# Kernel optimization log

Hardware: AMD Instinct MI355X
Metric: run time of the kernel (lower is better)

Reference implementation:

```python
import jax, jax.numpy as jnp
import numpy as np

C, H, W = 3, 2048, 2048
N_ANN = 64
P = 512  # patch resolution
RESIZE_FRAC = 0.5  # deterministic midpoint of resize_range=(0.25, 0.75)
MIN_SIZE = 10


def setup_inputs() -> dict:
    key = jax.random.key(0)
    k1, k2, k3, k4 = jax.random.split(key, 4)
    image = jax.random.normal(k1, (C, H, W), jnp.float32)
    patch = jax.random.uniform(k2, (C, P, P), jnp.float32)
    # build valid normalized xyxy boxes (x1<x2, y1<y2) inside the image
    centers = jax.random.uniform(k3, (N_ANN, 2), minval=0.2, maxval=0.8)
    sizes = jax.random.uniform(k4, (N_ANN, 2), minval=0.10, maxval=0.30)
    xy1 = jnp.clip(centers - sizes / 2, 0.0, 1.0)
    xy2 = jnp.clip(centers + sizes / 2, 0.0, 1.0)
    annotations = jnp.concatenate([xy1, xy2], axis=1).astype(jnp.float32)  # [N,4] xyxy
    return {"image": image, "annotations": annotations, "patch": patch}


def reference(image, annotations, patch):
    """MODE_CENTER_BBOX forward: for each bbox, bilinearly resize the patch to
    wh x wh (wh = min(bbox_w, bbox_h) * RESIZE_FRAC, >= MIN_SIZE), then paste it
    centered in the bbox (clamped to the image). embed_patch's mask arithmetic
    (image_mask*image + patch_mask*patch) is exactly a region overwrite."""
    c, h, w = image.shape
    # normalized_annotations=True: scale by [W, H, W, H] then floor to long
    ann = np.asarray(annotations * jnp.array([w, h, w, h], jnp.float32)).astype(np.int64)
    img = image
    for x1, y1, x2, y2 in ann:
        bw, bh = int(x2 - x1), int(y2 - y1)
        wh = max(int(min(bw, bh) * RESIZE_FRAC), MIN_SIZE)
        rp = jax.image.resize(patch, (c, wh, wh), method="bilinear")
        x = int(x1) + bw // 2 - wh // 2
        y = int(y1) + bh // 2 - wh // 2
        y = max(min(h - wh, y), 0)
        x = max(min(w - wh, x), 0)
        img = img.at[:, y:y + wh, x:x + wh].set(rp)
    return img
```

## Files before the change

### kernel.cpp

```cpp
#include <hip/hip_runtime.h>

#define CCH 3
#define HH 2048
#define WW 2048
#define NANN 64
#define PSZ 512
#define HWIMG (HH * WW)
#define PP (PSZ * PSZ)
#define WHMAX 308
#define OYB 4
#define CHS ((size_t)PSZ * WHMAX)
#define GX (WW / 256)
#define GY (HH / 4)
#define NTILE (GX * GY)

__global__ void prep_kernel(const float* __restrict__ ann, int* __restrict__ meta) {
    int a = threadIdx.x;
    if (a >= NANN) return;
    float x1f = ann[a * 4 + 0] * (float)WW;
    float y1f = ann[a * 4 + 1] * (float)HH;
    float x2f = ann[a * 4 + 2] * (float)WW;
    float y2f = ann[a * 4 + 3] * (float)HH;
    int x1 = (int)x1f, y1 = (int)y1f, x2 = (int)x2f, y2 = (int)y2f;
    int bw = x2 - x1, bh = y2 - y1;
    int mn = bw < bh ? bw : bh;
    int wh = mn / 2;
    if (wh < 10) wh = 10;
    int x = x1 + bw / 2 - wh / 2;
    int y = y1 + bh / 2 - wh / 2;
    y = min(HH - wh, y); y = max(y, 0);
    x = min(WW - wh, x); x = max(x, 0);
    meta[a * 4 + 0] = x;
    meta[a * 4 + 1] = y;
    meta[a * 4 + 2] = wh;
    meta[a * 4 + 3] = 0;
}

__global__ __launch_bounds__(256) void resize_y4_kernel(
    const float* __restrict__ patch, const int* __restrict__ meta,
    float* __restrict__ tmp)
{
    const int a   = blockIdx.y;
    const int oy0 = blockIdx.x * OYB;
    const int wh  = meta[a * 4 + 2];
    if (oy0 >= wh) return;

    const int xx = threadIdx.x * 2;
    const float inv = 512.0f / (float)wh;
    const float rs  = (float)wh / 512.0f;

    float syf[OYB];
#pragma unroll
    for (int i = 0; i < OYB; ++i)
        syf[i] = ((float)(oy0 + i) + 0.5f) * inv - 0.5f;

    const int ylast = min(oy0 + OYB - 1, wh - 1);
    const float syfL = ((float)ylast + 0.5f) * inv - 0.5f;
    const int ylo = max(0,       (int)ceilf(syf[0] - inv));
    const int yhi = min(PSZ - 1, (int)floorf(syfL + inv));

    float2 ac[OYB][3];
    float dy[OYB];
#pragma unroll
    for (int i = 0; i < OYB; ++i) {
        dy[i] = 0.f;
#pragma unroll
        for (int c = 0; c < 3; ++c) { ac[i][c].x = 0.f; ac[i][c].y = 0.f; }
    }

    const float* p = patch + xx;
#pragma unroll 2
    for (int yy = ylo; yy <= yhi; ++yy) {
        const float* row = p + yy * PSZ;
        float2 v0 = *(const float2*)(row);
        float2 v1 = *(const float2*)(row + PP);
        float2 v2 = *(const float2*)(row + 2 * PP);
#pragma unroll
        for (int i = 0; i < OYB; ++i) {
            float w = fmaxf(0.f, 1.f - fabsf(syf[i] - (float)yy) * rs);
            dy[i] += w;
            ac[i][0].x = fmaf(w, v0.x, ac[i][0].x);
            ac[i][0].y = fmaf(w, v0.y, ac[i][0].y);
            ac[i][1].x = fmaf(w, v1.x, ac[i][1].x);
            ac[i][1].y = fmaf(w, v1.y, ac[i][1].y);
            ac[i][2].x = fmaf(w, v2.x, ac[i][2].x);
            ac[i][2].y = fmaf(w, v2.y, ac[i][2].y);
        }
    }

#pragma unroll
    for (int i = 0; i < OYB; ++i) {
        int oy = oy0 + i;
        if (oy < wh) {
            float s = 1.0f / dy[i];
            float* t = tmp + ((size_t)(a * 3) * WHMAX + oy) * PSZ + xx;
            float2 o0 = { ac[i][0].x * s, ac[i][0].y * s };
            float2 o1 = { ac[i][1].x * s, ac[i][1].y * s };
            float2 o2 = { ac[i][2].x * s, ac[i][2].y * s };
            *(float2*)(t)           = o0;
            *(float2*)(t + CHS)     = o1;
            *(float2*)(t + 2 * CHS) = o2;
        }
    }
}

__device__ __forceinline__ void resample_px(
    const float* __restrict__ tmp, int a, int wh, int jx, int jy,
    float* __restrict__ out, int idx)
{
    const float inv = 512.0f / (float)wh;
    const float rs  = (float)wh / 512.0f;
    const float sxf = ((float)jx + 0.5f) * inv - 0.5f;
    const int xlo = max(0,       (int)ceilf(sxf - inv));
    const int xhi = min(PSZ - 1, (int)floorf(sxf + inv));

    const float* tb = tmp + ((size_t)(a * 3) * WHMAX + jy) * PSZ;
    float dx = 0.f, a0 = 0.f, a1 = 0.f, a2 = 0.f;

    const int ka = xlo & ~3;
    const int k8 = min(ka, 504);

    if (xhi - k8 <= 7) {
        float wgt[8];
#pragma unroll
        for (int j = 0; j < 8; ++j) {
            int pos = k8 + j;
            float w = (pos <= xhi) ? fmaxf(0.f, 1.f - fabsf(sxf - (float)pos) * rs) : 0.f;
            wgt[j] = w; dx += w;
        }
#pragma unroll
        for (int u = 0; u < 2; ++u) {
            float4 qa = *(const float4*)(tb + k8 + 4 * u);
            float4 qb = *(const float4*)(tb + CHS + k8 + 4 * u);
            float4 qc = *(const float4*)(tb + 2 * CHS + k8 + 4 * u);
            a0 = fmaf(wgt[4*u+0], qa.x, a0); a0 = fmaf(wgt[4*u+1], qa.y, a0);
            a0 = fmaf(wgt[4*u+2], qa.z, a0); a0 = fmaf(wgt[4*u+3], qa.w, a0);
            a1 = fmaf(wgt[4*u+0], qb.x, a1); a1 = fmaf(wgt[4*u+1], qb.y, a1);
            a1 = fmaf(wgt[4*u+2], qb.z, a1); a1 = fmaf(wgt[4*u+3], qb.w, a1);
            a2 = fmaf(wgt[4*u+0], qc.x, a2); a2 = fmaf(wgt[4*u+1], qc.y, a2);
            a2 = fmaf(wgt[4*u+2], qc.z, a2); a2 = fmaf(wgt[4*u+3], qc.w, a2);
        }
    } else {
        const int k16 = min(ka, 496);
        if (xhi - k16 <= 15) {
            float wgt[16];
#pragma unroll
            for (int j = 0; j < 16; ++j) {
                int pos = k16 + j;
                float w = (pos <= xhi) ? fmaxf(0.f, 1.f - fabsf(sxf - (float)pos) * rs) : 0.f;
                wgt[j] = w; dx += w;
            }
#pragma unroll
            for (int u = 0; u < 4; ++u) {
                float4 qa = *(const float4*)(tb + k16 + 4 * u);
                float4 qb = *(const float4*)(tb + CHS + k16 + 4 * u);
                float4 qc = *(const float4*)(tb + 2 * CHS + k16 + 4 * u);
                a0 = fmaf(wgt[4*u+0], qa.x, a0); a0 = fmaf(wgt[4*u+1], qa.y, a0);
                a0 = fmaf(wgt[4*u+2], qa.z, a0); a0 = fmaf(wgt[4*u+3], qa.w, a0);
                a1 = fmaf(wgt[4*u+0], qb.x, a1); a1 = fmaf(wgt[4*u+1], qb.y, a1);
                a1 = fmaf(wgt[4*u+2], qb.z, a1); a1 = fmaf(wgt[4*u+3], qb.w, a1);
                a2 = fmaf(wgt[4*u+0], qc.x, a2); a2 = fmaf(wgt[4*u+1], qc.y, a2);
                a2 = fmaf(wgt[4*u+2], qc.z, a2); a2 = fmaf(wgt[4*u+3], qc.w, a2);
            }
        } else {
            for (int x = xlo; x <= xhi; ++x)
                dx += fmaxf(0.f, 1.f - fabsf(sxf - (float)x) * rs);
            for (int x = xlo; x <= xhi; ++x) {
                float w = fmaxf(0.f, 1.f - fabsf(sxf - (float)x) * rs);
                a0 = fmaf(w, tb[x],           a0);
                a1 = fmaf(w, tb[x + CHS],     a1);
                a2 = fmaf(w, tb[x + 2 * CHS], a2);
            }
        }
    }
    const float s = 1.0f / dx;
    out[idx]             = a0 * s;
    out[idx + HWIMG]     = a1 * s;
    out[idx + 2 * HWIMG] = a2 * s;
}

__global__ __launch_bounds__(256) void composite_kernel(
    const float* __restrict__ img, const float* __restrict__ tmp,
    const int* __restrict__ meta, float* __restrict__ out)
{
    __shared__ int sax[NANN], say[NANN], sawh[NANN];
    __shared__ unsigned long long smask;

    const int tid = threadIdx.x;
    const int lid = blockIdx.y * GX + blockIdx.x;
    const int sid = (lid * 1543) & (NTILE - 1);
    const int bx = (sid & (GX - 1)) * 256;
    const int by = (sid / GX) * 4;

    if (tid < NANN) {
        int x = meta[tid * 4 + 0];
        int y = meta[tid * 4 + 1];
        int wh = meta[tid * 4 + 2];
        sax[tid] = x; say[tid] = y; sawh[tid] = wh;
        bool ov = (x < bx + 256) && (x + wh > bx) && (y < by + 4) && (y + wh > by);
        unsigned long long mm = __ballot(ov);
        if (tid == 0) smask = mm;
    }
    __syncthreads();

    const unsigned long long tmask = smask;

    if (tmask == 0) {
        const int x0  = bx + (tid & 63) * 4;
        const int py  = by + (tid >> 6);
        const int idx = py * WW + x0;
        *(float4*)(out + idx)             = *(const float4*)(img + idx);
        *(float4*)(out + idx + HWIMG)     = *(const float4*)(img + idx + HWIMG);
        *(float4*)(out + idx + 2 * HWIMG) = *(const float4*)(img + idx + 2 * HWIMG);
        return;
    }

    const int lx = tid & 63;
    const int py = by + (tid >> 6);
#pragma unroll
    for (int it = 0; it < 4; ++it) {
        const int px  = bx + it * 64 + lx;
        const int idx = py * WW + px;

        unsigned long long m = tmask;
        int hit = -1;
        while (m) {
            int a = 63 - __clzll(m);
            if (px >= sax[a] && px < sax[a] + sawh[a] &&
                py >= say[a] && py < say[a] + sawh[a]) { hit = a; break; }
            m &= ~(1ull << a);
        }

        if (hit < 0) {
            out[idx]             = img[idx];
            out[idx + HWIMG]     = img[idx + HWIMG];
            out[idx + 2 * HWIMG] = img[idx + 2 * HWIMG];
        } else {
            resample_px(tmp, hit, sawh[hit], px - sax[hit], py - say[hit], out, idx);
        }
    }
}

extern "C" void kernel_launch(void* const* d_in, const int* in_sizes, int n_in,
                              void* d_out, int out_size, void* d_ws, size_t ws_size,
                              hipStream_t stream) {
    const float* img   = (const float*)d_in[0];
    const float* ann   = (const float*)d_in[1];
    const float* patch = (const float*)d_in[2];
    float* out = (float*)d_out;

    int*   meta = (int*)d_ws;
    float* tmp  = (float*)((char*)d_ws + 4096);

    hipLaunchKernelGGL(prep_kernel, dim3(1), dim3(64), 0, stream, ann, meta);
    hipLaunchKernelGGL(resize_y4_kernel, dim3((WHMAX + OYB - 1) / OYB, NANN), dim3(256),
                       0, stream, patch, meta, tmp);
    hipLaunchKernelGGL(composite_kernel, dim3(GX, GY), dim3(256), 0, stream,
                       img, tmp, meta, out);
}
```

Before: 66.85 us.

## Store intermediate resized patches as bf16 and drop tile swizzle

The vertically resized intermediate buffer is now stored as bf16 with round-to-nearest instead of fp32, halving its write and read traffic. The horizontal resample reads eight bf16 values per 16-byte load, and a new 24-wide unrolled path replaces part of the scalar fallback. The composite kernel's pseudo-random tile remapping is removed in favour of a plain block mapping. This trades precision in the intermediate for bandwidth, which may exceed the output tolerance, and the plain tile order may worsen load balance across CUs.

```diff
diff --git a/kernel.cpp b/kernel.cpp
--- a/kernel.cpp
+++ b/kernel.cpp
@@ -9,10 +9,29 @@
 #define PP (PSZ * PSZ)
 #define WHMAX 308
 #define OYB 4
-#define CHS ((size_t)PSZ * WHMAX)
+#define CHSE ((size_t)PSZ * WHMAX)
 #define GX (WW / 256)
 #define GY (HH / 4)
-#define NTILE (GX * GY)
+
+typedef unsigned short u16;
+typedef unsigned int u32;
+
+__device__ __forceinline__ u16 f2bf(float f) {
+    u32 x = __float_as_uint(f);
+    x += 0x7FFFu + ((x >> 16) & 1u);
+    return (u16)(x >> 16);
+}
+
+__device__ __forceinline__ void acc8(const float* w, uint4 q, float& acc) {
+    acc = fmaf(w[0], __uint_as_float(q.x << 16),         acc);
+    acc = fmaf(w[1], __uint_as_float(q.x & 0xFFFF0000u), acc);
+    acc = fmaf(w[2], __uint_as_float(q.y << 16),         acc);
+    acc = fmaf(w[3], __uint_as_float(q.y & 0xFFFF0000u), acc);
+    acc = fmaf(w[4], __uint_as_float(q.z << 16),         acc);
+    acc = fmaf(w[5], __uint_as_float(q.z & 0xFFFF0000u), acc);
+    acc = fmaf(w[6], __uint_as_float(q.w << 16),         acc);
+    acc = fmaf(w[7], __uint_as_float(q.w & 0xFFFF0000u), acc);
+}
 
 __global__ void prep_kernel(const float* __restrict__ ann, int* __restrict__ meta) {
     int a = threadIdx.x;
@@ -38,7 +57,7 @@
 
 __global__ __launch_bounds__(256) void resize_y4_kernel(
     const float* __restrict__ patch, const int* __restrict__ meta,
-    float* __restrict__ tmp)
+    u16* __restrict__ tmp)
 {
     const int a   = blockIdx.y;
     const int oy0 = blockIdx.x * OYB;
@@ -93,19 +112,19 @@
         int oy = oy0 + i;
         if (oy < wh) {
             float s = 1.0f / dy[i];
-            float* t = tmp + ((size_t)(a * 3) * WHMAX + oy) * PSZ + xx;
-            float2 o0 = { ac[i][0].x * s, ac[i][0].y * s };
-            float2 o1 = { ac[i][1].x * s, ac[i][1].y * s };
-            float2 o2 = { ac[i][2].x * s, ac[i][2].y * s };
-            *(float2*)(t)           = o0;
-            *(float2*)(t + CHS)     = o1;
-            *(float2*)(t + 2 * CHS) = o2;
+            u16* t = tmp + ((size_t)(a * 3) * WHMAX + oy) * PSZ + xx;
+            ushort2 o0 = { f2bf(ac[i][0].x * s), f2bf(ac[i][0].y * s) };
+            ushort2 o1 = { f2bf(ac[i][1].x * s), f2bf(ac[i][1].y * s) };
+            ushort2 o2 = { f2bf(ac[i][2].x * s), f2bf(ac[i][2].y * s) };
+            *(ushort2*)(t)            = o0;
+            *(ushort2*)(t + CHSE)     = o1;
+            *(ushort2*)(t + 2 * CHSE) = o2;
         }
     }
 }
 
 __device__ __forceinline__ void resample_px(
-    const float* __restrict__ tmp, int a, int wh, int jx, int jy,
+    const u16* __restrict__ tmp, int a, int wh, int jx, int jy,
     float* __restrict__ out, int idx)
 {
     const float inv = 512.0f / (float)wh;
@@ -114,65 +133,64 @@
     const int xlo = max(0,       (int)ceilf(sxf - inv));
     const int xhi = min(PSZ - 1, (int)floorf(sxf + inv));
 
-    const float* tb = tmp + ((size_t)(a * 3) * WHMAX + jy) * PSZ;
+    const u16* tb = tmp + ((size_t)(a * 3) * WHMAX + jy) * PSZ;
+    const int k = xlo & ~7;
+    const int span = xhi - k;
+
     float dx = 0.f, a0 = 0.f, a1 = 0.f, a2 = 0.f;
 
-    const int ka = xlo & ~3;
-    const int k8 = min(ka, 504);
-
-    if (xhi - k8 <= 7) {
-        float wgt[8];
+    if (span <= 7) {
+        float w[8];
 #pragma unroll
         for (int j = 0; j < 8; ++j) {
-            int pos = k8 + j;
-            float w = (pos <= xhi) ? fmaxf(0.f, 1.f - fabsf(sxf - (float)pos) * rs) : 0.f;
-            wgt[j] = w; dx += w;
-        }
-#pragma unroll
-        for (int u = 0; u < 2; ++u) {
-            float4 qa = *(const float4*)(tb + k8 + 4 * u);
-            float4 qb = *(const float4*)(tb + CHS + k8 + 4 * u);
-            float4 qc = *(const float4*)(tb + 2 * CHS + k8 + 4 * u);
-            a0 = fmaf(wgt[4*u+0], qa.x, a0); a0 = fmaf(wgt[4*u+1], qa.y, a0);
-            a0 = fmaf(wgt[4*u+2], qa.z, a0); a0 = fmaf(wgt[4*u+3], qa.w, a0);
-            a1 = fmaf(wgt[4*u+0], qb.x, a1); a1 = fmaf(wgt[4*u+1], qb.y, a1);
-            a1 = fmaf(wgt[4*u+2], qb.z, a1); a1 = fmaf(wgt[4*u+3], qb.w, a1);
-            a2 = fmaf(wgt[4*u+0], qc.x, a2); a2 = fmaf(wgt[4*u+1], qc.y, a2);
-            a2 = fmaf(wgt[4*u+2], qc.z, a2); a2 = fmaf(wgt[4*u+3], qc.w, a2);
-        }
+            int pos = k + j;
+            float ww = (pos <= xhi) ? fmaxf(0.f, 1.f - fabsf(sxf - (float)pos) * rs) : 0.f;
+            w[j] = ww; dx += ww;
+        }
+        acc8(w, *(const uint4*)(tb + k),            a0);
+        acc8(w, *(const uint4*)(tb + CHSE + k),     a1);
+        acc8(w, *(const uint4*)(tb + 2 * CHSE + k), a2);
+    } else if (span <= 15) {
+        float w[16];
+#pragma unroll
+        for (int j = 0; j < 16; ++j) {
+            int pos = k + j;
+            float ww = (pos <= xhi) ? fmaxf(0.f, 1.f - fabsf(sxf - (float)pos) * rs) : 0.f;
+            w[j] = ww; dx += ww;
+        }
+        acc8(w,     *(const uint4*)(tb + k),                a0);
+        acc8(w + 8, *(const uint4*)(tb + k + 8),            a0);
+        acc8(w,     *(const uint4*)(tb + CHSE + k),         a1);
+        acc8(w + 8, *(const uint4*)(tb + CHSE + k + 8),     a1);
+        acc8(w,     *(const uint4*)(tb + 2 * CHSE + k),     a2);
+        acc8(w + 8, *(const uint4*)(tb + 2 * CHSE + k + 8), a2);
+    } else if (span <= 23) {
+        float w[24];
+#pragma unroll
+        for (int j = 0; j < 24; ++j) {
+            int pos = k + j;
+            float ww = (pos <= xhi) ? fmaxf(0.f, 1.f - fabsf(sxf - (float)pos) * rs) : 0.f;
+            w[j] = ww; dx += ww;
+        }
+        acc8(w,      *(const uint4*)(tb + k),                 a0);
+        acc8(w + 8,  *(const uint4*)(tb + k + 8),             a0);
+        acc8(w + 16, *(const uint4*)(tb + k + 16),            a0);
+        acc8(w,      *(const uint4*)(tb + CHSE + k),          a1);
+        acc8(w + 8,  *(const uint4*)(tb + CHSE + k + 8),      a1);
+        acc8(w + 16, *(const uint4*)(tb + CHSE + k + 16),     a1);
+        acc8(w,      *(const uint4*)(tb + 2 * CHSE + k),      a2);
+        acc8(w + 8,  *(const uint4*)(tb + 2 * CHSE + k + 8),  a2);
+        acc8(w + 16, *(const uint4*)(tb + 2 * CHSE + k + 16), a2);
     } else {
-        const int k16 = min(ka, 496);
-        if (xhi - k16 <= 15) {
-            float wgt[16];
-#pragma unroll
-            for (int j = 0; j < 16; ++j) {
-                int pos = k16 + j;
-                float w = (pos <= xhi) ? fmaxf(0.f, 1.f - fabsf(sxf - (float)pos) * rs) : 0.f;
-                wgt[j] = w; dx += w;
-            }
-#pragma unroll
-            for (int u = 0; u < 4; ++u) {
-                float4 qa = *(const float4*)(tb + k16 + 4 * u);
-                float4 qb = *(const float4*)(tb + CHS + k16 + 4 * u);
-                float4 qc = *(const float4*)(tb + 2 * CHS + k16 + 4 * u);
-                a0 = fmaf(wgt[4*u+0], qa.x, a0); a0 = fmaf(wgt[4*u+1], qa.y, a0);
-                a0 = fmaf(wgt[4*u+2], qa.z, a0); a0 = fmaf(wgt[4*u+3], qa.w, a0);
-                a1 = fmaf(wgt[4*u+0], qb.x, a1); a1 = fmaf(wgt[4*u+1], qb.y, a1);
-                a1 = fmaf(wgt[4*u+2], qb.z, a1); a1 = fmaf(wgt[4*u+3], qb.w, a1);
-                a2 = fmaf(wgt[4*u+0], qc.x, a2); a2 = fmaf(wgt[4*u+1], qc.y, a2);
-                a2 = fmaf(wgt[4*u+2], qc.z, a2); a2 = fmaf(wgt[4*u+3], qc.w, a2);
-            }
-        } else {
-            for (int x = xlo; x <= xhi; ++x)
-                dx += fmaxf(0.f, 1.f - fabsf(sxf - (float)x) * rs);
-            for (int x = xlo; x <= xhi; ++x) {
-                float w = fmaxf(0.f, 1.f - fabsf(sxf - (float)x) * rs);
-                a0 = fmaf(w, tb[x],           a0);
-                a1 = fmaf(w, tb[x + CHS],     a1);
-                a2 = fmaf(w, tb[x + 2 * CHS], a2);
-            }
-        }
-    }
+        for (int x = xlo; x <= xhi; ++x) {
+            float ww = fmaxf(0.f, 1.f - fabsf(sxf - (float)x) * rs);
+            dx += ww;
+            a0 = fmaf(ww, __uint_as_float(((u32)tb[x])            << 16), a0);
+            a1 = fmaf(ww, __uint_as_float(((u32)tb[x + CHSE])     << 16), a1);
+            a2 = fmaf(ww, __uint_as_float(((u32)tb[x + 2 * CHSE]) << 16), a2);
+        }
+    }
+
     const float s = 1.0f / dx;
     out[idx]             = a0 * s;
     out[idx + HWIMG]     = a1 * s;
@@ -180,17 +198,15 @@
 }
 
 __global__ __launch_bounds__(256) void composite_kernel(
-    const float* __restrict__ img, const float* __restrict__ tmp,
+    const float* __restrict__ img, const u16* __restrict__ tmp,
     const int* __restrict__ meta, float* __restrict__ out)
 {
     __shared__ int sax[NANN], say[NANN], sawh[NANN];
     __shared__ unsigned long long smask;
 
     const int tid = threadIdx.x;
-    const int lid = blockIdx.y * GX + blockIdx.x;
-    const int sid = (lid * 1543) & (NTILE - 1);
-    const int bx = (sid & (GX - 1)) * 256;
-    const int by = (sid / GX) * 4;
+    const int bx = blockIdx.x * 256;
+    const int by = blockIdx.y * 4;
 
     if (tid < NANN) {
         int x = meta[tid * 4 + 0];
@@ -249,8 +265,8 @@
     const float* patch = (const float*)d_in[2];
     float* out = (float*)d_out;
 
-    int*   meta = (int*)d_ws;
-    float* tmp  = (float*)((char*)d_ws + 4096);
+    int* meta = (int*)d_ws;
+    u16* tmp  = (u16*)((char*)d_ws + 4096);
 
     hipLaunchKernelGGL(prep_kernel, dim3(1), dim3(64), 0, stream, ann, meta);
     hipLaunchKernelGGL(resize_y4_kernel, dim3((WHMAX + OYB - 1) / OYB, NANN), dim3(256),
```

Result: no change. 66.00 us (-1.3%).
